# Kernel optimization log

Hardware: AMD Instinct MI355X
Metric: run time of the kernel (lower is better)

Reference implementation:

```python
import jax, jax.numpy as jnp
import numpy as np
from jax import lax

WIN = 7            # win_size
K = 0.03           # stability constant
COV_NORM = WIN * WIN / (WIN * WIN - 1.0)  # faithful: win_size**2 / (win_size**2 - 1)


def setup_inputs() -> dict:
    key = jax.random.key(0)
    kx, ky = jax.random.split(key)
    x = jax.random.normal(kx, (2, 4, 160, 160, 96), dtype=jnp.float32)
    y = jax.random.randint(ky, (2, 1, 160, 160, 96), 0, 4, dtype=jnp.int64)
    return {"x": x, "y": y}


def _box_mean(a):
    s = lax.reduce_window(a, jnp.array(0, a.dtype), lax.add,
                          (1, 1, WIN, WIN, WIN), (1, 1, 1, 1, 1), 'VALID')
    return s / jnp.asarray(WIN ** 3, a.dtype)


def reference(x, y):
    B, C, H, W, D = x.shape
    # one_hot(y, num_classes=C): (B,1,H,W,D) int -> (B,C,H,W,D) float
    y1 = jnp.moveaxis(jax.nn.one_hot(y[:, 0], C, dtype=x.dtype), -1, 1)
    xr = x.reshape(-1, 1, H, W, D)
    yr = y1.reshape(-1, 1, H, W, D)
    xr = xr * yr
    data_range = jnp.max(yr)
    xr = jax.nn.sigmoid(xr)
    c = (K * data_range) ** 2 / 2
    ux = _box_mean(xr)
    uy = _box_mean(yr)
    uxx = _box_mean(xr * xr)
    uyy = _box_mean(yr * yr)
    uxy = _box_mean(xr * yr)
    vx = COV_NORM * (uxx - ux * ux)
    vy = COV_NORM * (uyy - uy * uy)
    vxy = COV_NORM * (uxy - ux * uy)
    s_value = (vxy + c) / (vx * vy + c)
    return 1.0 - jnp.mean(s_value)
```

## Files before the change

### kernel.cpp

```cpp
#include <hip/hip_runtime.h>
#include <hip/hip_fp16.h>

#define WINS 7
#define H 160
#define W 160
#define DD 96
#define HO 154
#define WO 154
#define DOUT 90
#define CSTRIDE (H*W*DD)

#define TH 8
#define TW 8
#define TD 16
#define IH 14
#define IW 14
#define NCOL (IH * IW)
#define IDU 22
#define NDP 11
#define ID 24
#define NV 6
#define NITEMS (NCOL * NV)
#define HTILES 20
#define WTILES 20
#define DTILES 6
#define DPB2 26

struct alignas(8) Half4 { __half x, y, z, w; };

static __device__ __forceinline__ __half2 u2h(unsigned int a) {
    __half2 r; __builtin_memcpy(&r, &a, 4); return r;
}
static __device__ __forceinline__ unsigned int h2u(__half2 v) {
    unsigned int r; __builtin_memcpy(&r, &v, 4); return r;
}
static __device__ __forceinline__ void pmask(__half2 v, __half2& p, __half2& m) {
    const unsigned int bits = h2u(v);
    const unsigned int neg  = bits & 0x80008000u;
    const unsigned int full = (neg >> 15) * 0xFFFFu;
    p = u2h(bits & ~full);
    m = u2h(((~bits >> 15) & 0x00010001u) * 0x3C00u);
}

__device__ __forceinline__ float sval(float c0, float c1, float c2) {
    const float S_t  = c1 + 0.5f  * (343.0f - c0);
    const float S_t2 = c2 + 0.25f * (343.0f - c0);
    const float inv  = 1.0f / 343.0f;
    const float ux   = S_t  * inv;
    const float uy   = c0   * inv;
    const float uxx  = S_t2 * inv;
    const float uxy  = c1   * inv;
    const float covn = 49.0f / 48.0f;
    const float cc   = 0.00045f;
    const float vx  = covn * (uxx - ux * ux);
    const float vy  = covn * (uy  - uy * uy);
    const float vxy = covn * (uxy - ux * uy);
    return (vxy + cc) * __builtin_amdgcn_rcpf(vx * vy + cc);
}

__global__ __launch_bounds__(256)
void sigmoid_prepass(const float* __restrict__ x,
                     const int* __restrict__ y,
                     __half* __restrict__ xs,
                     double* __restrict__ acc) {
    if (blockIdx.x == 0 && blockIdx.y == 0 && threadIdx.x == 0) acc[0] = 0.0;
    const int b  = blockIdx.y;
    const int qv = blockIdx.x * 256 + threadIdx.x;
    const int off = 4 * qv;
    const int4 yv = *(const int4*)(y + (size_t)b * CSTRIDE + off);
#pragma unroll
    for (int c = 0; c < 4; c++) {
        const size_t xo = ((size_t)(b * 4 + c)) * CSTRIDE + off;
        const float4 xv = *(const float4*)(x + xo);
        const float s0 = 1.0f / (1.0f + __expf(-xv.x));
        const float s1 = 1.0f / (1.0f + __expf(-xv.y));
        const float s2 = 1.0f / (1.0f + __expf(-xv.z));
        const float s3 = 1.0f / (1.0f + __expf(-xv.w));
        Half4 hv;
        hv.x = __float2half((yv.x == c) ? s0 : -s0);
        hv.y = __float2half((yv.y == c) ? s1 : -s1);
        hv.z = __float2half((yv.z == c) ? s2 : -s2);
        hv.w = __float2half((yv.w == c) ? s3 : -s3);
        *(Half4*)(xs + xo) = hv;
    }
}

template <bool PRE>
__global__ __launch_bounds__(256, 5)
void structure_loss_main(const float* __restrict__ x,
                         const int* __restrict__ y,
                         const __half* __restrict__ xs,
                         double* __restrict__ acc) {
    __shared__ __half sA0[IH * TW * IDU];
    __shared__ __half sA1[IH * TW * IDU];
    __shared__ __half sA2[IH * TW * IDU];
    __shared__ union alignas(16) {
        __half vs[NCOL * ID];
        struct {
            __half b0[TH * TW * DPB2];
            __half b1[TH * TW * DPB2];
            __half b2[TH * TW * DPB2];
        } sb;
    } u;
    __shared__ unsigned int yb[NCOL * 2];
    __shared__ float wsum[4];

    const int dt = blockIdx.x;
    const int wt = blockIdx.y;
    const int z  = blockIdx.z;
    const int b  = z / HTILES;
    const int ht = z - b * HTILES;

    const int h0 = ht * TH, w0 = wt * TW, d0 = dt * TD;
    const int* yc = y + (size_t)b * (size_t)CSTRIDE;
    const int t = threadIdx.x;

    if (!PRE) {
        for (int i = t; i < NCOL * 2; i += 256) {
            const int col = i >> 1, hf = i & 1;
            const int ih = col / IW, iw = col - ih * IW;
            const int h = min(h0 + ih, H - 1);
            const int w = min(w0 + iw, W - 1);
            const size_t cb = (size_t)(h * W + w) * DD;
            const int dstart = d0 + 12 * hf;
            unsigned int pk = 0u;
#pragma unroll
            for (int j3 = 0; j3 < 3; j3++) {
                const int dbase = dstart + 4 * j3;
                if (dbase < DD) {
                    const int4 yv = *(const int4*)(yc + cb + dbase);
                    pk |= (unsigned)(yv.x & 3) << (2 * (4 * j3 + 0));
                    pk |= (unsigned)(yv.y & 3) << (2 * (4 * j3 + 1));
                    pk |= (unsigned)(yv.z & 3) << (2 * (4 * j3 + 2));
                    pk |= (unsigned)(yv.w & 3) << (2 * (4 * j3 + 3));
                }
            }
            yb[i] = pk;
        }
        __syncthreads();
    }

    float lsum = 0.f;

    for (int cl = 0; cl < 4; cl++) {
        if (PRE) {
            const __half* xsc = xs + ((size_t)b * 4 + cl) * (size_t)CSTRIDE;
#pragma unroll
            for (int k = 0; k < 3; k++) {
                const int i = t + 256 * k;
                if (i < NCOL * 3) {
                    const int col = i / 3, q = i - col * 3;
                    const int ih = col / IW, iw = col - ih * IW;
                    const int h = min(h0 + ih, H - 1);
                    const int w = min(w0 + iw, W - 1);
                    const int dbase = d0 + 8 * q;
                    uint4 vv = make_uint4(0u, 0u, 0u, 0u);
                    if (dbase < DD)
                        vv = *(const uint4*)(xsc + (h * W + w) * DD + dbase);
                    *(uint4*)&u.vs[col * ID + 8 * q] = vv;
                }
            }
        } else {
            const float* xc = x + ((size_t)b * 4 + cl) * (size_t)CSTRIDE;
#pragma unroll
            for (int k = 0; k < 5; k++) {
                const int i = t + 256 * k;
                if (i < NITEMS) {
                    const int col = i / NV, q = i - col * NV;
                    const int ih = col / IW, iw = col - ih * IW;
                    const int h = min(h0 + ih, H - 1);
                    const int w = min(w0 + iw, W - 1);
                    const int dbase = d0 + 4 * q;
                    Half4 hv;
                    hv.x = hv.y = hv.z = hv.w = __float2half(0.f);
                    if (dbase < DD) {
                        const float4 xv = *(const float4*)(xc + (h * W + w) * DD + dbase);
                        const int wsel = (q >= 3) ? 1 : 0;
                        const unsigned int pk =
                            yb[col * 2 + wsel] >> (8 * (q - 3 * wsel));
                        const float s0 = 1.0f / (1.0f + __expf(-xv.x));
                        const float s1 = 1.0f / (1.0f + __expf(-xv.y));
                        const float s2 = 1.0f / (1.0f + __expf(-xv.z));
                        const float s3 = 1.0f / (1.0f + __expf(-xv.w));
                        hv.x = __float2half(((int)((pk >> 0) & 3u) == cl) ? s0 : -s0);
                        hv.y = __float2half(((int)((pk >> 2) & 3u) == cl) ? s1 : -s1);
                        hv.z = __float2half(((int)((pk >> 4) & 3u) == cl) ? s2 : -s2);
                        hv.w = __float2half(((int)((pk >> 6) & 3u) == cl) ? s3 : -s3);
                    }
                    *(Half4*)&u.vs[col * ID + 4 * q] = hv;
                }
            }
        }
        __syncthreads();

        if (t < IH * NDP) {
            const int ih = t / NDP, dp = t - ih * NDP;
            const int dd = 2 * dp;
            const __half2 z2 = __float2half2_rn(0.f);
            __half2 v2[IW];
            const int vbase = ih * IW * ID + dd;
#pragma unroll
            for (int iw = 0; iw < IW; iw++)
                v2[iw] = *(const __half2*)&u.vs[vbase + iw * ID];
            __half2 sm = z2, sp = z2, sq = z2;
#pragma unroll
            for (int iw = 0; iw < WINS; iw++) {
                __half2 p, m;
                pmask(v2[iw], p, m);
                sm = __hadd2(sm, m);
                sp = __hadd2(sp, p);
                sq = __hfma2(p, v2[iw], sq);
            }
            int o = (ih * TW) * IDU + dd;
            *(__half2*)&sA0[o] = sm;
            *(__half2*)&sA1[o] = sp;
            *(__half2*)&sA2[o] = sq;
#pragma unroll
            for (int wo = 1; wo < TW; wo++) {
                const __half2 a = v2[wo + 6], bb = v2[wo - 1];
                __half2 pa, ma, pb, mb;
                pmask(a, pa, ma);
                pmask(bb, pb, mb);
                sm = __hadd2(sm, __hsub2(ma, mb));
                sp = __hadd2(sp, __hsub2(pa, pb));
                sq = __hadd2(sq, __hsub2(__hmul2(pa, a), __hmul2(pb, bb)));
                o += IDU;
                *(__half2*)&sA0[o] = sm;
                *(__half2*)&sA1[o] = sp;
                *(__half2*)&sA2[o] = sq;
            }
        }
        __syncthreads();

        if (t < 2 * TW * NDP) {
            const int dp = t % NDP;
            const int r  = t / NDP;
            const int wo = r & 7;
            const int ho0 = (r >> 3) * 4;
            const int dd = 2 * dp;
            __half2 a0[10], a1[10], a2[10];
#pragma unroll
            for (int k = 0; k < 10; k++) {
                const int idx = ((ho0 + k) * TW + wo) * IDU + dd;
                a0[k] = *(const __half2*)&sA0[idx];
                a1[k] = *(const __half2*)&sA1[idx];
                a2[k] = *(const __half2*)&sA2[idx];
            }
            __half2 s0 = a0[0], s1 = a1[0], s2 = a2[0];
#pragma unroll
            for (int k = 1; k < WINS; k++) {
                s0 = __hadd2(s0, a0[k]);
                s1 = __hadd2(s1, a1[k]);
                s2 = __hadd2(s2, a2[k]);
            }
            int o = (ho0 * TW + wo) * DPB2 + dd;
            *(__half2*)&u.sb.b0[o] = s0;
            *(__half2*)&u.sb.b1[o] = s1;
            *(__half2*)&u.sb.b2[o] = s2;
#pragma unroll
            for (int k = 1; k < 4; k++) {
                s0 = __hadd2(s0, __hsub2(a0[k + 6], a0[k - 1]));
                s1 = __hadd2(s1, __hsub2(a1[k + 6], a1[k - 1]));
                s2 = __hadd2(s2, __hsub2(a2[k + 6], a2[k - 1]));
                o += TW * DPB2;
                *(__half2*)&u.sb.b0[o] = s0;
                *(__half2*)&u.sb.b1[o] = s1;
                *(__half2*)&u.sb.b2[o] = s2;
            }
        }
        __syncthreads();

        {
            const int dq = t & 3;
            const int wo = (t >> 2) & 7;
            const int ho = t >> 5;
            const int hg = h0 + ho, wg = w0 + wo;
            if (hg < HO && wg < WO) {
                const int base = (ho * TW + wo) * DPB2 + dq * 4;
                float b0[10], b1[10], b2[10];
#pragma unroll
                for (int k = 0; k < 5; k++) {
                    float2 f;
                    f = __half22float2(*(const __half2*)&u.sb.b0[base + 2 * k]);
                    b0[2 * k] = f.x; b0[2 * k + 1] = f.y;
                    f = __half22float2(*(const __half2*)&u.sb.b1[base + 2 * k]);
                    b1[2 * k] = f.x; b1[2 * k + 1] = f.y;
                    f = __half22float2(*(const __half2*)&u.sb.b2[base + 2 * k]);
                    b2[2 * k] = f.x; b2[2 * k + 1] = f.y;
                }
                float s0 = 0.f, s1 = 0.f, s2 = 0.f;
#pragma unroll
                for (int k = 0; k < WINS; k++) { s0 += b0[k]; s1 += b1[k]; s2 += b2[k]; }
                const int dg = d0 + dq * 4;
#pragma unroll
                for (int k = 0; k < 4; k++) {
                    if (k > 0) {
                        s0 += b0[k + 6] - b0[k - 1];
                        s1 += b1[k + 6] - b1[k - 1];
                        s2 += b2[k + 6] - b2[k - 1];
                    }
                    if (dg + k < DOUT) lsum += sval(s0, s1, s2);
                }
            }
        }
        __syncthreads();
    }

#pragma unroll
    for (int off = 32; off > 0; off >>= 1) lsum += __shfl_down(lsum, off, 64);
    const int wave = t >> 6;
    if ((t & 63) == 0) wsum[wave] = lsum;
    __syncthreads();
    if (t == 0) {
        const float s = wsum[0] + wsum[1] + wsum[2] + wsum[3];
        atomicAdd(acc, (double)s);
    }
}

__global__ void structure_loss_finalize(const double* __restrict__ acc,
                                        float* __restrict__ out) {
    out[0] = 1.0f - (float)(acc[0] / 17075520.0);
}

extern "C" void kernel_launch(void* const* d_in, const int* in_sizes, int n_in,
                              void* d_out, int out_size, void* d_ws, size_t ws_size,
                              hipStream_t stream) {
    const float* x = (const float*)d_in[0];
    const int*   y = (const int*)d_in[1];
    double* acc = (double*)d_ws;
    __half* xs = (__half*)((char*)d_ws + 16);

    const size_t need = 16 + (size_t)8 * CSTRIDE * sizeof(__half);
    dim3 grid(DTILES, WTILES, 2 * HTILES);

    if (ws_size >= need) {
        sigmoid_prepass<<<dim3(2400, 2), 256, 0, stream>>>(x, y, xs, acc);
        structure_loss_main<true><<<grid, 256, 0, stream>>>(x, y, xs, acc);
    } else {
        (void)hipMemsetAsync(d_ws, 0, sizeof(double), stream);
        structure_loss_main<false><<<grid, 256, 0, stream>>>(x, y, xs, acc);
    }
    structure_loss_finalize<<<1, 1, 0, stream>>>(acc, (float*)d_out);
}
```

Baseline: 209.6 us.

## Enlarge depth tile to 24 outputs and interleave partial-sum shared layout

Raises the per-block depth tile from 16 to 24 outputs, cutting the grid's depth tiles from 6 to 4. Fewer tiles means less redundant halo loading and sigmoid work per output. The last tile is staged from a clamped depth offset so all global loads stay in bounds without branches. The stage-2 partial sums now use an interleaved half2 layout with an odd stride, meant to reduce LDS bank conflicts. The cost is more shared memory and more registers per thread, which may lower occupancy under launch_bounds(256,5).

```diff
diff --git a/kernel.cpp b/kernel.cpp
--- a/kernel.cpp
+++ b/kernel.cpp
@@ -12,19 +12,19 @@
 
 #define TH 8
 #define TW 8
-#define TD 16
+#define TD 24
 #define IH 14
 #define IW 14
 #define NCOL (IH * IW)
-#define IDU 22
-#define NDP 11
-#define ID 24
-#define NV 6
-#define NITEMS (NCOL * NV)
+#define IDS 32
+#define IDW 30
+#define NDP 15
+#define SAS 30
+#define SBC 49
 #define HTILES 20
 #define WTILES 20
-#define DTILES 6
-#define DPB2 26
+#define DTILES 4
+
 
 struct alignas(8) Half4 { __half x, y, z, w; };
 
@@ -91,18 +91,14 @@
                          const int* __restrict__ y,
                          const __half* __restrict__ xs,
                          double* __restrict__ acc) {
-    __shared__ __half sA0[IH * TW * IDU];
-    __shared__ __half sA1[IH * TW * IDU];
-    __shared__ __half sA2[IH * TW * IDU];
+    __shared__ __half sA0[IH * TW * SAS];
+    __shared__ __half sA1[IH * TW * SAS];
+    __shared__ __half sA2[IH * TW * SAS];
     __shared__ union alignas(16) {
-        __half vs[NCOL * ID];
-        struct {
-            __half b0[TH * TW * DPB2];
-            __half b1[TH * TW * DPB2];
-            __half b2[TH * TW * DPB2];
-        } sb;
+        __half  vs[NCOL * IDS];
+        __half2 sb2[64 * SBC + 3];
     } u;
-    __shared__ unsigned int yb[NCOL * 2];
+    __shared__ unsigned int yb[PRE ? 1 : NCOL * 2];
     __shared__ float wsum[4];
 
     const int dt = blockIdx.x;
@@ -111,7 +107,11 @@
     const int b  = z / HTILES;
     const int ht = z - b * HTILES;
 
-    const int h0 = ht * TH, w0 = wt * TW, d0 = dt * TD;
+    const int h0 = ht * TH, w0 = wt * TW;
+    const int d0 = dt * TD;
+    const int dstage = (dt == DTILES - 1) ? 64 : d0;
+    const int doff = d0 - dstage;
+    const int odmax = min(TD, DOUT - d0);
     const int* yc = y + (size_t)b * (size_t)CSTRIDE;
     const int t = threadIdx.x;
 
@@ -122,18 +122,15 @@
             const int h = min(h0 + ih, H - 1);
             const int w = min(w0 + iw, W - 1);
             const size_t cb = (size_t)(h * W + w) * DD;
-            const int dstart = d0 + 12 * hf;
+            const int dstart = dstage + 16 * hf;
             unsigned int pk = 0u;
 #pragma unroll
-            for (int j3 = 0; j3 < 3; j3++) {
-                const int dbase = dstart + 4 * j3;
-                if (dbase < DD) {
-                    const int4 yv = *(const int4*)(yc + cb + dbase);
-                    pk |= (unsigned)(yv.x & 3) << (2 * (4 * j3 + 0));
-                    pk |= (unsigned)(yv.y & 3) << (2 * (4 * j3 + 1));
-                    pk |= (unsigned)(yv.z & 3) << (2 * (4 * j3 + 2));
-                    pk |= (unsigned)(yv.w & 3) << (2 * (4 * j3 + 3));
-                }
+            for (int j3 = 0; j3 < 4; j3++) {
+                const int4 yv = *(const int4*)(yc + cb + dstart + 4 * j3);
+                pk |= (unsigned)(yv.x & 3) << (2 * (4 * j3 + 0));
+                pk |= (unsigned)(yv.y & 3) << (2 * (4 * j3 + 1));
+                pk |= (unsigned)(yv.z & 3) << (2 * (4 * j3 + 2));
+                pk |= (unsigned)(yv.w & 3) << (2 * (4 * j3 + 3));
             }
             yb[i] = pk;
         }
@@ -146,48 +143,41 @@
         if (PRE) {
             const __half* xsc = xs + ((size_t)b * 4 + cl) * (size_t)CSTRIDE;
 #pragma unroll
-            for (int k = 0; k < 3; k++) {
+            for (int k = 0; k < 4; k++) {
                 const int i = t + 256 * k;
-                if (i < NCOL * 3) {
-                    const int col = i / 3, q = i - col * 3;
+                if (i < NCOL * 4) {
+                    const int col = i >> 2, q = i & 3;
                     const int ih = col / IW, iw = col - ih * IW;
                     const int h = min(h0 + ih, H - 1);
                     const int w = min(w0 + iw, W - 1);
-                    const int dbase = d0 + 8 * q;
-                    uint4 vv = make_uint4(0u, 0u, 0u, 0u);
-                    if (dbase < DD)
-                        vv = *(const uint4*)(xsc + (h * W + w) * DD + dbase);
-                    *(uint4*)&u.vs[col * ID + 8 * q] = vv;
+                    const uint4 vv =
+                        *(const uint4*)(xsc + (h * W + w) * DD + dstage + 8 * q);
+                    *(uint4*)&u.vs[col * IDS + 8 * q] = vv;
                 }
             }
         } else {
             const float* xc = x + ((size_t)b * 4 + cl) * (size_t)CSTRIDE;
 #pragma unroll
-            for (int k = 0; k < 5; k++) {
+            for (int k = 0; k < 7; k++) {
                 const int i = t + 256 * k;
-                if (i < NITEMS) {
-                    const int col = i / NV, q = i - col * NV;
+                if (i < NCOL * 8) {
+                    const int col = i >> 3, q = i & 7;
                     const int ih = col / IW, iw = col - ih * IW;
                     const int h = min(h0 + ih, H - 1);
                     const int w = min(w0 + iw, W - 1);
-                    const int dbase = d0 + 4 * q;
+                    const int dbase = dstage + 4 * q;
+                    const float4 xv = *(const float4*)(xc + (h * W + w) * DD + dbase);
+                    const unsigned int pk = yb[col * 2 + (q >> 2)] >> (8 * (q & 3));
+                    const float s0 = 1.0f / (1.0f + __expf(-xv.x));
+                    const float s1 = 1.0f / (1.0f + __expf(-xv.y));
+                    const float s2 = 1.0f / (1.0f + __expf(-xv.z));
+                    const float s3 = 1.0f / (1.0f + __expf(-xv.w));
                     Half4 hv;
-                    hv.x = hv.y = hv.z = hv.w = __float2half(0.f);
-                    if (dbase < DD) {
-                        const float4 xv = *(const float4*)(xc + (h * W + w) * DD + dbase);
-                        const int wsel = (q >= 3) ? 1 : 0;
-                        const unsigned int pk =
-                            yb[col * 2 + wsel] >> (8 * (q - 3 * wsel));
-                        const float s0 = 1.0f / (1.0f + __expf(-xv.x));
-                        const float s1 = 1.0f / (1.0f + __expf(-xv.y));
-                        const float s2 = 1.0f / (1.0f + __expf(-xv.z));
-                        const float s3 = 1.0f / (1.0f + __expf(-xv.w));
-                        hv.x = __float2half(((int)((pk >> 0) & 3u) == cl) ? s0 : -s0);
-                        hv.y = __float2half(((int)((pk >> 2) & 3u) == cl) ? s1 : -s1);
-                        hv.z = __float2half(((int)((pk >> 4) & 3u) == cl) ? s2 : -s2);
-                        hv.w = __float2half(((int)((pk >> 6) & 3u) == cl) ? s3 : -s3);
-                    }
-                    *(Half4*)&u.vs[col * ID + 4 * q] = hv;
+                    hv.x = __float2half(((int)((pk >> 0) & 3u) == cl) ? s0 : -s0);
+                    hv.y = __float2half(((int)((pk >> 2) & 3u) == cl) ? s1 : -s1);
+                    hv.z = __float2half(((int)((pk >> 4) & 3u) == cl) ? s2 : -s2);
+                    hv.w = __float2half(((int)((pk >> 6) & 3u) == cl) ? s3 : -s3);
+                    *(Half4*)&u.vs[col * IDS + 4 * q] = hv;
                 }
             }
         }
@@ -195,13 +185,13 @@
 
         if (t < IH * NDP) {
             const int ih = t / NDP, dp = t - ih * NDP;
-            const int dd = 2 * dp;
+            const int s  = min(doff + 2 * dp, IDS - 2);
             const __half2 z2 = __float2half2_rn(0.f);
             __half2 v2[IW];
-            const int vbase = ih * IW * ID + dd;
+            const int vbase = ih * IW * IDS + s;
 #pragma unroll
             for (int iw = 0; iw < IW; iw++)
-                v2[iw] = *(const __half2*)&u.vs[vbase + iw * ID];
+                v2[iw] = *(const __half2*)&u.vs[vbase + iw * IDS];
             __half2 sm = z2, sp = z2, sq = z2;
 #pragma unroll
             for (int iw = 0; iw < WINS; iw++) {
@@ -211,7 +201,7 @@
                 sp = __hadd2(sp, p);
                 sq = __hfma2(p, v2[iw], sq);
             }
-            int o = (ih * TW) * IDU + dd;
+            int o = (ih * TW) * SAS + 2 * dp;
             *(__half2*)&sA0[o] = sm;
             *(__half2*)&sA1[o] = sp;
             *(__half2*)&sA2[o] = sq;
@@ -224,7 +214,7 @@
                 sm = __hadd2(sm, __hsub2(ma, mb));
                 sp = __hadd2(sp, __hsub2(pa, pb));
                 sq = __hadd2(sq, __hsub2(__hmul2(pa, a), __hmul2(pb, bb)));
-                o += IDU;
+                o += SAS;
                 *(__half2*)&sA0[o] = sm;
                 *(__half2*)&sA1[o] = sp;
                 *(__half2*)&sA2[o] = sq;
@@ -237,11 +227,10 @@
             const int r  = t / NDP;
             const int wo = r & 7;
             const int ho0 = (r >> 3) * 4;
-            const int dd = 2 * dp;
             __half2 a0[10], a1[10], a2[10];
 #pragma unroll
             for (int k = 0; k < 10; k++) {
-                const int idx = ((ho0 + k) * TW + wo) * IDU + dd;
+                const int idx = ((ho0 + k) * TW + wo) * SAS + 2 * dp;
                 a0[k] = *(const __half2*)&sA0[idx];
                 a1[k] = *(const __half2*)&sA1[idx];
                 a2[k] = *(const __half2*)&sA2[idx];
@@ -253,19 +242,15 @@
                 s1 = __hadd2(s1, a1[k]);
                 s2 = __hadd2(s2, a2[k]);
             }
-            int o = (ho0 * TW + wo) * DPB2 + dd;
-            *(__half2*)&u.sb.b0[o] = s0;
-            *(__half2*)&u.sb.b1[o] = s1;
-            *(__half2*)&u.sb.b2[o] = s2;
+            int o = ((ho0 * TW + wo) * SBC) + dp * 3;
+            u.sb2[o] = s0; u.sb2[o + 1] = s1; u.sb2[o + 2] = s2;
 #pragma unroll
             for (int k = 1; k < 4; k++) {
                 s0 = __hadd2(s0, __hsub2(a0[k + 6], a0[k - 1]));
                 s1 = __hadd2(s1, __hsub2(a1[k + 6], a1[k - 1]));
                 s2 = __hadd2(s2, __hsub2(a2[k + 6], a2[k - 1]));
-                o += TW * DPB2;
-                *(__half2*)&u.sb.b0[o] = s0;
-                *(__half2*)&u.sb.b1[o] = s1;
-                *(__half2*)&u.sb.b2[o] = s2;
+                o += TW * SBC;
+                u.sb2[o] = s0; u.sb2[o + 1] = s1; u.sb2[o + 2] = s2;
             }
         }
         __syncthreads();
@@ -276,30 +261,30 @@
             const int ho = t >> 5;
             const int hg = h0 + ho, wg = w0 + wo;
             if (hg < HO && wg < WO) {
-                const int base = (ho * TW + wo) * DPB2 + dq * 4;
-                float b0[10], b1[10], b2[10];
-#pragma unroll
-                for (int k = 0; k < 5; k++) {
+                const int base2 = (ho * TW + wo) * SBC + 9 * dq;
+                float b0[12], b1[12], b2[12];
+#pragma unroll
+                for (int k = 0; k < 6; k++) {
                     float2 f;
-                    f = __half22float2(*(const __half2*)&u.sb.b0[base + 2 * k]);
+                    f = __half22float2(u.sb2[base2 + 3 * k + 0]);
                     b0[2 * k] = f.x; b0[2 * k + 1] = f.y;
-                    f = __half22float2(*(const __half2*)&u.sb.b1[base + 2 * k]);
+                    f = __half22float2(u.sb2[base2 + 3 * k + 1]);
                     b1[2 * k] = f.x; b1[2 * k + 1] = f.y;
-                    f = __half22float2(*(const __half2*)&u.sb.b2[base + 2 * k]);
+                    f = __half22float2(u.sb2[base2 + 3 * k + 2]);
                     b2[2 * k] = f.x; b2[2 * k + 1] = f.y;
                 }
                 float s0 = 0.f, s1 = 0.f, s2 = 0.f;
 #pragma unroll
                 for (int k = 0; k < WINS; k++) { s0 += b0[k]; s1 += b1[k]; s2 += b2[k]; }
-                const int dg = d0 + dq * 4;
-#pragma unroll
-                for (int k = 0; k < 4; k++) {
+                const int od0 = 6 * dq;
+#pragma unroll
+                for (int k = 0; k < 6; k++) {
                     if (k > 0) {
                         s0 += b0[k + 6] - b0[k - 1];
                         s1 += b1[k + 6] - b1[k - 1];
                         s2 += b2[k + 6] - b2[k - 1];
                     }
-                    if (dg + k < DOUT) lsum += sval(s0, s1, s2);
+                    if (od0 + k < odmax) lsum += sval(s0, s1, s2);
                 }
             }
         }
```

Measured after the change: 199.3 us. 1.05x faster.
